# Kernel tuning notes

Hardware: AMD Instinct MI355X
Metric: run time of the kernel (lower is better)

Reference implementation:

```python
import jax, jax.numpy as jnp
import numpy as np

NUM_HEADS = 16
HIDDEN = 1024
HEAD_DIM = HIDDEN // NUM_HEADS
B, S, D = 2, 2048, 1024


def setup_inputs() -> dict:
    key = jax.random.key(0)
    ks = jax.random.split(key, 7)
    scale = 1.0 / np.sqrt(D)
    return {
        "query": jax.random.normal(ks[0], (B, S, D), dtype=jnp.float32),
        "key": jax.random.normal(ks[1], (B, S, D), dtype=jnp.float32),
        "value": jax.random.normal(ks[2], (B, S, D), dtype=jnp.float32),
        "Wk_w": jax.random.normal(ks[3], (HIDDEN, D), dtype=jnp.float32) * scale,
        "Wk_b": jax.random.normal(ks[4], (HIDDEN,), dtype=jnp.float32) * scale,
        "Wv_w": jax.random.normal(ks[5], (HIDDEN, D), dtype=jnp.float32) * scale,
        "Wv_b": jax.random.normal(ks[6], (HIDDEN,), dtype=jnp.float32) * scale,
    }


def reference(query, key, value, Wk_w, Wk_b, Wv_w, Wv_b):
    # NOTE: in the original torch module, self.W_v is assigned twice, so the
    # SAME Linear (Wv) projects both key and value; Wk projects query.
    b, s, _ = query.shape

    def split_heads(x):  # [b,s,hidden] -> [b,h,s,hd]
        return x.reshape(b, s, NUM_HEADS, HEAD_DIM).transpose(0, 2, 1, 3)

    q = split_heads(query @ Wk_w.T + Wk_b)
    k = split_heads(key @ Wv_w.T + Wv_b)
    v = split_heads(value @ Wv_w.T + Wv_b)

    scores = jnp.einsum("bhqd,bhkd->bhqk", q, k) / jnp.sqrt(
        jnp.asarray(HEAD_DIM, dtype=q.dtype))
    probs = jax.nn.softmax(scores, axis=-1)
    out = jnp.einsum("bhqk,bhkd->bhqd", probs, v)
    return out.transpose(0, 2, 1, 3).reshape(b, s, NUM_HEADS * HEAD_DIM)
```

## Files before the change

kernel.cpp:

```cpp
#include <hip/hip_runtime.h>
#include <stdint.h>

typedef unsigned short u16;
typedef uint32_t u32;
typedef __bf16 bf16x8 __attribute__((ext_vector_type(8)));
typedef float f32x4 __attribute__((ext_vector_type(4)));
typedef float f32x16 __attribute__((ext_vector_type(16)));
typedef u16 u16x4 __attribute__((ext_vector_type(4)));
typedef u16 u16x8 __attribute__((ext_vector_type(8)));

#define XQ_OFF 0ul
#define XK_OFF 4194304ul
#define XV_OFF 8388608ul
#define WK_OFF 12582912ul
#define WV_OFF 13631488ul
#define Q_OFF  14680064ul
#define K_OFF  18874368ul
#define V_OFF  23068672ul

#define SCQ 0.18033688011112042f

#if __has_builtin(__builtin_amdgcn_exp2f)
#define EXP2F(x) __builtin_amdgcn_exp2f(x)
#else
#define EXP2F(x) exp2f(x)
#endif

__device__ __forceinline__ u16 f2bf(float f) {
  u32 u = __float_as_uint(f);
  u32 r = (u + 0x7fffu + ((u >> 16) & 1u)) >> 16;
  return (u16)r;
}

__device__ __forceinline__ u32 pk2(float a, float b) {
  typedef __bf16 bf2_t __attribute__((ext_vector_type(2)));
  typedef float f2_t __attribute__((ext_vector_type(2)));
  f2_t v; v[0] = a; v[1] = b;
  bf2_t h = __builtin_convertvector(v, bf2_t);
  union { bf2_t h; u32 u; } cv; cv.h = h; return cv.u;
}

__device__ __forceinline__ void load_lds16(const void* g, void* l) {
  __builtin_amdgcn_global_load_lds(
      (const __attribute__((address_space(1))) u32*)g,
      (__attribute__((address_space(3))) u32*)l, 16, 0, 0);
}

__device__ __forceinline__ u32 swz(u32 L) {
  return L ^ (((L >> 7) & 1u) << 4) ^ (((L >> 10) & 3u) << 5);
}

__global__ __launch_bounds__(256) void cvt_tile_kernel(
    const float* __restrict__ xq, const float* __restrict__ xk,
    const float* __restrict__ xv, const float* __restrict__ wk,
    const float* __restrict__ wv, u16* __restrict__ ws) {
  __shared__ u16 tile[4096];
  const int bid = blockIdx.x;
  const float* src; size_t dstbase; int rt, ktp;
  if (bid < 3072) {
    int m = bid >> 10, loc = bid & 1023;
    src = (m == 0) ? xq : (m == 1) ? xk : xv;
    dstbase = (size_t)m * 4194304ul;
    rt = loc >> 4; ktp = loc & 15;
  } else {
    int r2 = bid - 3072;
    int m = r2 >> 8, loc = r2 & 255;
    src = m ? wv : wk;
    dstbase = WK_OFF + (size_t)m * 1048576ul;
    rt = loc >> 4; ktp = loc & 15;
  }
  const int t = threadIdx.x;
  const int row0 = t >> 4, c = t & 15;
  const int k = c * 4;
  const float* s = src + (size_t)(rt * 64 + row0) * 1024ul + ktp * 64 + k;
#pragma unroll
  for (int i = 0; i < 4; ++i) {
    float4 v = *(const float4*)(s + (size_t)i * 16384ul);
    int row = row0 + i * 16;
    u32* p = (u32*)(tile + ((k >> 5) * 2048 + ((k >> 3) & 3) * 512 + row * 8 + (k & 7)));
    p[0] = pk2(v.x, v.y);
    p[1] = pk2(v.z, v.w);
  }
  __syncthreads();
  u16* dst = ws + dstbase + (size_t)(rt * 32 + ktp * 2) * 2048ul;
#pragma unroll
  for (int so = 0; so < 4096; so += 2048)
    *(u16x8*)(dst + so + t * 8) = *(const u16x8*)(tile + so + t * 8);
}

__global__ __launch_bounds__(256, 3) void proj_kernel(u16* __restrict__ ws,
                                                      const float* __restrict__ bk,
                                                      const float* __restrict__ bv) {
  const int proj = blockIdx.z;
  const int mtile = blockIdx.x;
  const int ntile = blockIdx.y;
  const u16* A = ws + (size_t)proj * 4194304ul;
  const u16* Bw = ws + ((proj == 0) ? WK_OFF : WV_OFF);
  const float* bias = (proj == 0) ? bk : bv;
  u16* outQ = ws + Q_OFF;
  u16* outK = ws + K_OFF;
  u16* outV = ws + V_OFF;

  const int t = threadIdx.x;
  const int w = t >> 6, lane = t & 63;
  const int wm = w >> 1, wn = w & 1;
  const int g = lane >> 4, c = lane & 15;

  __shared__ __align__(16) u16 smem[24576];

  const u16* Ag = A + (size_t)(2 * mtile) * 65536ul;
  const u16* Bg = Bw + (size_t)(2 * ntile) * 65536ul;
  const u32 t8 = (u32)t * 8u;
  const u32 so = swz((u32)t * 16u) >> 1;

  u32 poff[4];
#pragma unroll
  for (int mt = 0; mt < 4; ++mt)
    poff[mt] = swz((u32)((g << 10) | ((mt * 16 + c) << 4))) >> 1;

#define PSTAGE(buf, kt)                                            \
  do {                                                             \
    u16* bb = smem + (buf) * 8192;                                 \
    const size_t ko = (size_t)(kt) * 2048ul + so;                  \
    load_lds16(Ag + ko, bb + t8);                                  \
    load_lds16(Ag + 65536ul + ko, bb + 2048 + t8);                 \
    load_lds16(Bg + ko, bb + 4096 + t8);                           \
    load_lds16(Bg + 65536ul + ko, bb + 6144 + t8);                 \
  } while (0)

#define PFRAGS_MFMA(buf)                                                        \
  do {                                                                          \
    const u16* Ap = smem + (buf) * 8192 + wm * 2048;                            \
    const u16* Bp = smem + (buf) * 8192 + 4096 + wn * 2048;                     \
    bf16x8 af[4], bfv[4];                                                       \
    _Pragma("unroll") for (int mt = 0; mt < 4; ++mt)                            \
        af[mt] = *(const bf16x8*)(Ap + poff[mt]);                               \
    _Pragma("unroll") for (int nt = 0; nt < 4; ++nt)                            \
        bfv[nt] = *(const bf16x8*)(Bp + poff[nt]);                              \
    _Pragma("unroll") for (int mt = 0; mt < 4; ++mt)                            \
        _Pragma("unroll") for (int nt = 0; nt < 4; ++nt)                        \
            acc[mt][nt] = __builtin_amdgcn_mfma_f32_16x16x32_bf16(              \
                af[mt], bfv[nt], acc[mt][nt], 0, 0, 0);                         \
  } while (0)

  f32x4 acc[4][4];
#pragma unroll
  for (int mt = 0; mt < 4; ++mt)
#pragma unroll
    for (int nt = 0; nt < 4; ++nt) acc[mt][nt] = (f32x4){0.f, 0.f, 0.f, 0.f};

  PSTAGE(0, 0);
  PSTAGE(1, 1);

  int cur = 0, stg = 2;
#pragma unroll 1
  for (int kt = 0; kt < 31; ++kt) {
    asm volatile("s_waitcnt vmcnt(4)\n\ts_barrier" ::: "memory");
    if (kt < 30) PSTAGE(stg, kt + 2);
    PFRAGS_MFMA(cur);
    cur = (cur == 2) ? 0 : cur + 1;
    stg = (stg == 2) ? 0 : stg + 1;
  }
  asm volatile("s_waitcnt vmcnt(0)\n\ts_barrier" ::: "memory");
  PFRAGS_MFMA(cur);
#undef PSTAGE
#undef PFRAGS_MFMA

  const int m0 = mtile * 128 + wm * 64;
  const int n0 = ntile * 128 + wn * 64;
  if (proj == 2) {
#pragma unroll
    for (int nt = 0; nt < 4; ++nt) {
      const int col = n0 + nt * 16 + c;
      const float bvv = bias[col];
      const int h = col >> 6, d = col & 63;
#pragma unroll
      for (int mt = 0; mt < 4; ++mt) {
        const int mbase = m0 + mt * 16 + g * 4;
        const int b = mbase >> 11;
        const int bh = b * 16 + h;
        const int s = mbase & 2047;
        u16x4 pk;
#pragma unroll
        for (int r = 0; r < 4; ++r) pk[r] = f2bf(acc[mt][nt][r] + bvv);
        size_t idx = (size_t)bh * 131072ul + (size_t)(s >> 6) * 4096ul +
                     (size_t)((s & 63) >> 3) * 512ul + (size_t)d * 8ul + (size_t)(s & 7);
        *(u16x4*)(outV + idx) = pk;
      }
    }
  } else {
    __syncthreads();
    u16* Ew = smem + w * 4096;
#pragma unroll
    for (int nt = 0; nt < 4; ++nt) {
      const int d = nt * 16 + c;
      const float bvv = bias[n0 + nt * 16 + c];
#pragma unroll
      for (int mt = 0; mt < 4; ++mt) {
#pragma unroll
        for (int r = 0; r < 4; ++r) {
          const int srow = mt * 16 + g * 4 + r;
          float y = acc[mt][nt][r] + bvv;
          if (proj == 0) y *= SCQ;
          Ew[(d >> 3) * 512 + srow * 8 + (d & 7)] = f2bf(y);
        }
      }
    }
    __syncthreads();
    const int b = mtile >> 4;
    const int bh = b * 16 + ntile * 2 + wn;
    if (proj == 0) {
      u16* base = outQ + (size_t)bh * 131072ul + (size_t)(mtile & 15) * 8192ul + wm * 512;
#pragma unroll
      for (int i = 0; i < 8; ++i)
        *(u16x8*)(base + i * 1024 + lane * 8) = *(const u16x8*)(Ew + i * 512 + lane * 8);
    } else {
      u16* base = outK + (size_t)bh * 131072ul + (size_t)((mtile & 15) * 2 + wm) * 4096ul;
#pragma unroll
      for (int i = 0; i < 8; ++i)
        *(u16x8*)(base + i * 512 + lane * 8) = *(const u16x8*)(Ew + i * 512 + lane * 8);
    }
  }
}

__global__ __launch_bounds__(256, 2) void attn_kernel(const u16* __restrict__ ws,
                                                      float* __restrict__ out) {
  const int bh = blockIdx.x, qtile = blockIdx.y;
  const int b = bh >> 4, h = bh & 15;
  const int t = threadIdx.x, w = t >> 6, lane = t & 63;
  const int c32 = lane & 31, g2 = lane >> 5;

  __shared__ __align__(16) u16 Ks[3][4096];
  __shared__ __align__(16) u16 Vs[3][4096];

  const u16* Qg = ws + Q_OFF + (size_t)bh * 131072ul + (size_t)qtile * 8192ul;
  const u16* Kg = ws + K_OFF + (size_t)bh * 131072ul;
  const u16* Vg = ws + V_OFF + (size_t)bh * 131072ul;

  bf16x8 qf[4];
#pragma unroll
  for (int ks = 0; ks < 4; ++ks)
    qf[ks] = *(const bf16x8*)(Qg + (size_t)(ks * 2 + g2) * 1024ul +
                              (size_t)(w * 32 + c32) * 8ul);

  f32x16 O0, O1, Lacc;
#pragma unroll
  for (int i = 0; i < 16; ++i) { O0[i] = 0.f; O1[i] = 0.f; Lacc[i] = 0.f; }

#define STAGE_KV(buf, jj)                                        \
  do {                                                           \
    const u16* Kj = Kg + (size_t)(jj) * 4096ul;                  \
    const u16* Vj = Vg + (size_t)(jj) * 4096ul;                  \
    load_lds16(Kj + (size_t)t * 8ul, &Ks[buf][t * 8]);           \
    load_lds16(Kj + 2048ul + (size_t)t * 8ul, &Ks[buf][2048 + t * 8]); \
    load_lds16(Vj + (size_t)t * 8ul, &Vs[buf][t * 8]);           \
    load_lds16(Vj + 2048ul + (size_t)t * 8ul, &Vs[buf][2048 + t * 8]); \
  } while (0)

  STAGE_KV(0, 0);
  STAGE_KV(1, 1);

  int buf = 0;
#pragma unroll 1
  for (int j = 0; j < 32; ++j) {
    asm volatile("s_waitcnt vmcnt(4)\n\ts_barrier" ::: "memory");
    const u16* Kb = Ks[buf];
    const u16* Vb = Vs[buf];
    {
      int jc = (j + 2 < 32) ? j + 2 : 31;
      int sb = buf - 1; if (sb < 0) sb += 3;
      STAGE_KV(sb, jc);
    }

    f32x16 S0, S1;
#pragma unroll
    for (int i = 0; i < 16; ++i) { S0[i] = 0.f; S1[i] = 0.f; }
    __builtin_amdgcn_s_setprio(1);
#pragma unroll
    for (int ks = 0; ks < 4; ++ks) {
      bf16x8 kf0 = *(const bf16x8*)(Kb + (ks * 2 + g2) * 512 + c32 * 8);
      bf16x8 kf1 = *(const bf16x8*)(Kb + (ks * 2 + g2) * 512 + (32 + c32) * 8);
      S0 = __builtin_amdgcn_mfma_f32_32x32x16_bf16(kf0, qf[ks], S0, 0, 0, 0);
      S1 = __builtin_amdgcn_mfma_f32_32x32x16_bf16(kf1, qf[ks], S1, 0, 0, 0);
    }
    __builtin_amdgcn_s_setprio(0);

#pragma unroll
    for (int i = 0; i < 16; ++i) { S0[i] = EXP2F(S0[i]); S1[i] = EXP2F(S1[i]); }
    Lacc += S0;
    Lacc += S1;

    u32 pa[4][4];
#pragma unroll
    for (int half = 0; half < 2; ++half) {
      const f32x16& Sx = half ? S1 : S0;
#pragma unroll
      for (int sub = 0; sub < 2; ++sub) {
        const int rb = sub * 8;
        u32 a0 = pk2(Sx[rb + 0], Sx[rb + 1]);
        u32 a1 = pk2(Sx[rb + 2], Sx[rb + 3]);
        u32 a2 = pk2(Sx[rb + 4], Sx[rb + 5]);
        u32 a3 = pk2(Sx[rb + 6], Sx[rb + 7]);
        asm volatile("v_permlane32_swap_b32 %0, %1" : "+v"(a0), "+v"(a2));
        asm volatile("v_permlane32_swap_b32 %0, %1" : "+v"(a1), "+v"(a3));
        const int kstep = half * 2 + sub;
        pa[kstep][0] = a0; pa[kstep][1] = a1; pa[kstep][2] = a2; pa[kstep][3] = a3;
      }
    }

    __builtin_amdgcn_s_setprio(1);
#pragma unroll
    for (int kstep = 0; kstep < 4; ++kstep) {
      union { u32 u[4]; bf16x8 b; } pcv;
#pragma unroll
      for (int i = 0; i < 4; ++i) pcv.u[i] = pa[kstep][i];
      bf16x8 vf0 = *(const bf16x8*)(Vb + (kstep * 2 + g2) * 512 + c32 * 8);
      bf16x8 vf1 = *(const bf16x8*)(Vb + (kstep * 2 + g2) * 512 + (32 + c32) * 8);
      O0 = __builtin_amdgcn_mfma_f32_32x32x16_bf16(pcv.b, vf0, O0, 0, 0, 0);
      O1 = __builtin_amdgcn_mfma_f32_32x32x16_bf16(pcv.b, vf1, O1, 0, 0, 0);
    }
    __builtin_amdgcn_s_setprio(0);

    buf = (buf == 2) ? 0 : buf + 1;
  }
#undef STAGE_KV

  float lp = 0.f;
#pragma unroll
  for (int i = 0; i < 16; ++i) lp += Lacc[i];
  float lA = lp, lB = lp;
  asm volatile("v_permlane32_swap_b32 %0, %1" : "+v"(lA), "+v"(lB));
  const float Ltot = lA + lB;

  const int q0 = qtile * 128 + w * 32;
  float* outb = out + (size_t)(b * 2048 + q0) * 1024ul + h * 64 + c32;
#pragma unroll
  for (int r = 0; r < 16; ++r) {
    const int qr = (r & 3) + 8 * (r >> 2) + 4 * g2;
    int lv = __builtin_amdgcn_ds_bpermute(qr << 2, __float_as_int(Ltot));
    const float inv = 1.0f / __int_as_float(lv);
    float* rp = outb + (size_t)qr * 1024ul;
    rp[0] = O0[r] * inv;
    rp[32] = O1[r] * inv;
  }
}

extern "C" void kernel_launch(void* const* d_in, const int* in_sizes, int n_in,
                              void* d_out, int out_size, void* d_ws, size_t ws_size,
                              hipStream_t stream) {
  const float* q = (const float*)d_in[0];
  const float* k = (const float*)d_in[1];
  const float* v = (const float*)d_in[2];
  const float* wk = (const float*)d_in[3];
  const float* bk = (const float*)d_in[4];
  const float* wv = (const float*)d_in[5];
  const float* bv = (const float*)d_in[6];
  u16* ws = (u16*)d_ws;
  float* out = (float*)d_out;

  cvt_tile_kernel<<<3584, 256, 0, stream>>>(q, k, v, wk, wv, ws);
  proj_kernel<<<dim3(32, 8, 3), 256, 0, stream>>>(ws, bk, bv);
  attn_kernel<<<dim3(32, 16), 256, 0, stream>>>(ws, out);
}
```

Measured before the change: 177.1 us.

## Fuse fp32-to-bf16 conversion into projection GEMM, drop separate convert kernel

Removes the standalone conversion kernel that wrote bf16 tiled copies of the inputs and weights into the workspace. The projection GEMM now loads fp32 rows directly into registers, converts them to bf16 and stores them swizzled into LDS, with register prefetch and an LDS double buffer instead of the three-stage async global-to-LDS pipeline. This saves one launch plus a full write and re-read of the converted activations. In exchange, conversion work is repeated across tiles: each weight tile is converted once per m-tile, and each activation tile once per n-tile. Global loads also become synchronous register loads.

Result: slower. 203.1 us (+14.7%).

```diff
diff --git a/kernel.cpp b/kernel.cpp
--- a/kernel.cpp
+++ b/kernel.cpp
@@ -8,12 +8,8 @@
 typedef float f32x16 __attribute__((ext_vector_type(16)));
 typedef u16 u16x4 __attribute__((ext_vector_type(4)));
 typedef u16 u16x8 __attribute__((ext_vector_type(8)));
-
-#define XQ_OFF 0ul
-#define XK_OFF 4194304ul
-#define XV_OFF 8388608ul
-#define WK_OFF 12582912ul
-#define WV_OFF 13631488ul
+typedef u32 u32x4 __attribute__((ext_vector_type(4)));
+
 #define Q_OFF  14680064ul
 #define K_OFF  18874368ul
 #define V_OFF  23068672ul
@@ -50,52 +46,16 @@
   return L ^ (((L >> 7) & 1u) << 4) ^ (((L >> 10) & 3u) << 5);
 }
 
-__global__ __launch_bounds__(256) void cvt_tile_kernel(
+__global__ __launch_bounds__(256, 3) void proj_kernel(
     const float* __restrict__ xq, const float* __restrict__ xk,
     const float* __restrict__ xv, const float* __restrict__ wk,
-    const float* __restrict__ wv, u16* __restrict__ ws) {
-  __shared__ u16 tile[4096];
-  const int bid = blockIdx.x;
-  const float* src; size_t dstbase; int rt, ktp;
-  if (bid < 3072) {
-    int m = bid >> 10, loc = bid & 1023;
-    src = (m == 0) ? xq : (m == 1) ? xk : xv;
-    dstbase = (size_t)m * 4194304ul;
-    rt = loc >> 4; ktp = loc & 15;
-  } else {
-    int r2 = bid - 3072;
-    int m = r2 >> 8, loc = r2 & 255;
-    src = m ? wv : wk;
-    dstbase = WK_OFF + (size_t)m * 1048576ul;
-    rt = loc >> 4; ktp = loc & 15;
-  }
-  const int t = threadIdx.x;
-  const int row0 = t >> 4, c = t & 15;
-  const int k = c * 4;
-  const float* s = src + (size_t)(rt * 64 + row0) * 1024ul + ktp * 64 + k;
-#pragma unroll
-  for (int i = 0; i < 4; ++i) {
-    float4 v = *(const float4*)(s + (size_t)i * 16384ul);
-    int row = row0 + i * 16;
-    u32* p = (u32*)(tile + ((k >> 5) * 2048 + ((k >> 3) & 3) * 512 + row * 8 + (k & 7)));
-    p[0] = pk2(v.x, v.y);
-    p[1] = pk2(v.z, v.w);
-  }
-  __syncthreads();
-  u16* dst = ws + dstbase + (size_t)(rt * 32 + ktp * 2) * 2048ul;
-#pragma unroll
-  for (int so = 0; so < 4096; so += 2048)
-    *(u16x8*)(dst + so + t * 8) = *(const u16x8*)(tile + so + t * 8);
-}
-
-__global__ __launch_bounds__(256, 3) void proj_kernel(u16* __restrict__ ws,
-                                                      const float* __restrict__ bk,
-                                                      const float* __restrict__ bv) {
+    const float* __restrict__ wv, const float* __restrict__ bk,
+    const float* __restrict__ bv, u16* __restrict__ ws) {
   const int proj = blockIdx.z;
   const int mtile = blockIdx.x;
   const int ntile = blockIdx.y;
-  const u16* A = ws + (size_t)proj * 4194304ul;
-  const u16* Bw = ws + ((proj == 0) ? WK_OFF : WV_OFF);
+  const float* xa = (proj == 0) ? xq : (proj == 1) ? xk : xv;
+  const float* wsrc = (proj == 0) ? wk : wv;
   const float* bias = (proj == 0) ? bk : bv;
   u16* outQ = ws + Q_OFF;
   u16* outK = ws + K_OFF;
@@ -106,26 +66,53 @@
   const int wm = w >> 1, wn = w & 1;
   const int g = lane >> 4, c = lane & 15;
 
-  __shared__ __align__(16) u16 smem[24576];
-
-  const u16* Ag = A + (size_t)(2 * mtile) * 65536ul;
-  const u16* Bg = Bw + (size_t)(2 * ntile) * 65536ul;
-  const u32 t8 = (u32)t * 8u;
-  const u32 so = swz((u32)t * 16u) >> 1;
+  __shared__ __align__(16) u16 smem[16384];
+
+  const int sr = (t >> 1) & 63;
+  const int sh = t >> 7;
+  const int scp = t & 1;
+  const float* Asrc = xa + (size_t)(mtile * 128 + sh * 64 + sr) * 1024ul + scp * 16;
+  const float* Bsrc = wsrc + (size_t)(ntile * 128 + sh * 64 + sr) * 1024ul + scp * 16;
+  const u32 wo0 = (u32)sh * 2048u + (swz((u32)(scp * 2 + 0) * 1024u + (u32)sr * 16u) >> 1);
+  const u32 wo1 = (u32)sh * 2048u + (swz((u32)(scp * 2 + 1) * 1024u + (u32)sr * 16u) >> 1);
 
   u32 poff[4];
 #pragma unroll
   for (int mt = 0; mt < 4; ++mt)
     poff[mt] = swz((u32)((g << 10) | ((mt * 16 + c) << 4))) >> 1;
 
-#define PSTAGE(buf, kt)                                            \
-  do {                                                             \
-    u16* bb = smem + (buf) * 8192;                                 \
-    const size_t ko = (size_t)(kt) * 2048ul + so;                  \
-    load_lds16(Ag + ko, bb + t8);                                  \
-    load_lds16(Ag + 65536ul + ko, bb + 2048 + t8);                 \
-    load_lds16(Bg + ko, bb + 4096 + t8);                           \
-    load_lds16(Bg + 65536ul + ko, bb + 6144 + t8);                 \
+  float4 a0, a1, a2, a3, b0, b1, b2, b3;
+
+#define ISSUE(kt)                                         \
+  do {                                                    \
+    const float* ap_ = Asrc + (size_t)(kt) * 32ul;        \
+    const float* bp_ = Bsrc + (size_t)(kt) * 32ul;        \
+    a0 = *(const float4*)(ap_ + 0);                       \
+    a1 = *(const float4*)(ap_ + 4);                       \
+    a2 = *(const float4*)(ap_ + 8);                       \
+    a3 = *(const float4*)(ap_ + 12);                      \
+    b0 = *(const float4*)(bp_ + 0);                       \
+    b1 = *(const float4*)(bp_ + 4);                       \
+    b2 = *(const float4*)(bp_ + 8);                       \
+    b3 = *(const float4*)(bp_ + 12);                      \
+  } while (0)
+
+#define CVTW(buf)                                                   \
+  do {                                                              \
+    u16* Ab_ = smem + (buf) * 8192;                                 \
+    u32x4 vA0, vA1, vB0, vB1;                                       \
+    vA0[0] = pk2(a0.x, a0.y); vA0[1] = pk2(a0.z, a0.w);             \
+    vA0[2] = pk2(a1.x, a1.y); vA0[3] = pk2(a1.z, a1.w);             \
+    vA1[0] = pk2(a2.x, a2.y); vA1[1] = pk2(a2.z, a2.w);             \
+    vA1[2] = pk2(a3.x, a3.y); vA1[3] = pk2(a3.z, a3.w);             \
+    vB0[0] = pk2(b0.x, b0.y); vB0[1] = pk2(b0.z, b0.w);             \
+    vB0[2] = pk2(b1.x, b1.y); vB0[3] = pk2(b1.z, b1.w);             \
+    vB1[0] = pk2(b2.x, b2.y); vB1[1] = pk2(b2.z, b2.w);             \
+    vB1[2] = pk2(b3.x, b3.y); vB1[3] = pk2(b3.z, b3.w);             \
+    *(u32x4*)(Ab_ + wo0) = vA0;                                     \
+    *(u32x4*)(Ab_ + wo1) = vA1;                                     \
+    *(u32x4*)(Ab_ + 4096 + wo0) = vB0;                              \
+    *(u32x4*)(Ab_ + 4096 + wo1) = vB1;                              \
   } while (0)
 
 #define PFRAGS_MFMA(buf)                                                        \
@@ -149,21 +136,22 @@
 #pragma unroll
     for (int nt = 0; nt < 4; ++nt) acc[mt][nt] = (f32x4){0.f, 0.f, 0.f, 0.f};
 
-  PSTAGE(0, 0);
-  PSTAGE(1, 1);
-
-  int cur = 0, stg = 2;
+  ISSUE(0);
+  CVTW(0);
+  ISSUE(1);
+  asm volatile("s_waitcnt lgkmcnt(0)\n\ts_barrier" ::: "memory");
+
 #pragma unroll 1
-  for (int kt = 0; kt < 31; ++kt) {
-    asm volatile("s_waitcnt vmcnt(4)\n\ts_barrier" ::: "memory");
-    if (kt < 30) PSTAGE(stg, kt + 2);
-    PFRAGS_MFMA(cur);
-    cur = (cur == 2) ? 0 : cur + 1;
-    stg = (stg == 2) ? 0 : stg + 1;
+  for (int kt = 0; kt < 32; ++kt) {
+    PFRAGS_MFMA(kt & 1);
+    if (kt < 31) {
+      CVTW((kt + 1) & 1);
+      if (kt < 30) ISSUE(kt + 2);
+      asm volatile("s_waitcnt lgkmcnt(0)\n\ts_barrier" ::: "memory");
+    }
   }
-  asm volatile("s_waitcnt vmcnt(0)\n\ts_barrier" ::: "memory");
-  PFRAGS_MFMA(cur);
-#undef PSTAGE
+#undef ISSUE
+#undef CVTW
 #undef PFRAGS_MFMA
 
   const int m0 = mtile * 128 + wm * 64;
@@ -297,14 +285,14 @@
 #pragma unroll
       for (int sub = 0; sub < 2; ++sub) {
         const int rb = sub * 8;
-        u32 a0 = pk2(Sx[rb + 0], Sx[rb + 1]);
-        u32 a1 = pk2(Sx[rb + 2], Sx[rb + 3]);
-        u32 a2 = pk2(Sx[rb + 4], Sx[rb + 5]);
-        u32 a3 = pk2(Sx[rb + 6], Sx[rb + 7]);
-        asm volatile("v_permlane32_swap_b32 %0, %1" : "+v"(a0), "+v"(a2));
-        asm volatile("v_permlane32_swap_b32 %0, %1" : "+v"(a1), "+v"(a3));
+        u32 q0 = pk2(Sx[rb + 0], Sx[rb + 1]);
+        u32 q1 = pk2(Sx[rb + 2], Sx[rb + 3]);
+        u32 q2 = pk2(Sx[rb + 4], Sx[rb + 5]);
+        u32 q3 = pk2(Sx[rb + 6], Sx[rb + 7]);
+        asm volatile("v_permlane32_swap_b32 %0, %1" : "+v"(q0), "+v"(q2));
+        asm volatile("v_permlane32_swap_b32 %0, %1" : "+v"(q1), "+v"(q3));
         const int kstep = half * 2 + sub;
-        pa[kstep][0] = a0; pa[kstep][1] = a1; pa[kstep][2] = a2; pa[kstep][3] = a3;
+        pa[kstep][0] = q0; pa[kstep][1] = q1; pa[kstep][2] = q2; pa[kstep][3] = q3;
       }
     }
 
@@ -358,7 +346,6 @@
   u16* ws = (u16*)d_ws;
   float* out = (float*)d_out;
 
-  cvt_tile_kernel<<<3584, 256, 0, stream>>>(q, k, v, wk, wv, ws);
-  proj_kernel<<<dim3(32, 8, 3), 256, 0, stream>>>(ws, bk, bv);
+  proj_kernel<<<dim3(32, 8, 3), 256, 0, stream>>>(q, k, v, wk, wv, bk, bv, ws);
   attn_kernel<<<dim3(32, 16), 256, 0, stream>>>(ws, out);
 }
```
